# Kernel optimization log

Measured on AMD Instinct MI355X. Metric: run time of the kernel, lower is better.

Reference implementation:

```python
import jax, jax.numpy as jnp
import numpy as np

EPS = 1e-12


def conv3(x, W, b):
    # x: [B,C,H,W], W: [O,I,3,3] -> SAME conv, stride 1
    y = jax.lax.conv_general_dilated(x, W, (1, 1), 'SAME',
                                     dimension_numbers=('NCHW', 'OIHW', 'NCHW'))
    return y + b[None, :, None, None]


def unfold3(x):
    # torch F.unfold(kernel=3, padding=1): [B,C,H,W] -> [B, C*9, H*W]
    B, C, H, W = x.shape
    xp = jnp.pad(x, ((0, 0), (0, 0), (1, 1), (1, 1)))
    patches = jnp.stack([xp[:, :, i:i + H, j:j + W]
                         for i in range(3) for j in range(3)], axis=2)  # [B,C,9,H,W]
    return patches.reshape(B, C * 9, H * W)


def fold3(u, H, W):
    # torch F.fold(kernel=3, padding=1): [B, C*9, H*W] -> [B,C,H,W] (overlap-add)
    B = u.shape[0]
    C = u.shape[1] // 9
    p = u.reshape(B, C, 3, 3, H, W)
    out = jnp.zeros((B, C, H + 2, W + 2), u.dtype)
    for i in range(3):
        for j in range(3):
            out = out.at[:, :, i:i + H, j:j + W].add(p[:, :, i, j])
    return out[:, :, 1:-1, 1:-1]


def l2norm(v, axis):
    n = jnp.sqrt(jnp.sum(v * v, axis=axis, keepdims=True))
    return v / jnp.maximum(n, EPS)


def setup_inputs() -> dict:
    key = jax.random.key(0)
    ks = jax.random.split(key, 10)
    in_c, q_c = 64, 32
    B, H, W = 1, 96, 96
    s = 0.05
    return {
        'x':  jax.random.normal(ks[0], (B, in_c, H, W), jnp.float32),
        'W1': jax.random.normal(ks[1], (in_c, in_c, 3, 3), jnp.float32) * s,
        'b1': jax.random.normal(ks[2], (in_c,), jnp.float32) * s,
        'W2': jax.random.normal(ks[3], (in_c, in_c, 3, 3), jnp.float32) * s,
        'b2': jax.random.normal(ks[4], (in_c,), jnp.float32) * s,
        'Wq': jax.random.normal(ks[5], (q_c, in_c, 3, 3), jnp.float32) * s,
        'bq': jax.random.normal(ks[6], (q_c,), jnp.float32) * s,
        'Wk': jax.random.normal(ks[7], (q_c, in_c, 3, 3), jnp.float32) * s,
        'bk': jax.random.normal(ks[8], (q_c,), jnp.float32) * s,
    }


def reference(x, W1, b1, W2, b2, Wq, bq, Wk, bk):
    TOPK = 5
    B, C, H, W = x.shape
    L = H * W

    feature = jax.nn.relu(conv3(jax.nn.relu(conv3(x, W1, b1)), W2, b2))
    q = conv3(x, Wq, bq)
    k = conv3(x, Wk, bk)

    q_unfold = l2norm(unfold3(q), axis=1)                      # [B, Q9, L]
    k_unfold = l2norm(jnp.swapaxes(unfold3(k), 1, 2), axis=2)  # [B, L, Q9]

    R_qk = jnp.einsum('blc,bcm->blm', k_unfold, q_unfold)      # [B, L_k, L_q]

    # topk over dim=1 (key positions) for each query position
    vals, idxs = jax.lax.top_k(jnp.swapaxes(R_qk, 1, 2), TOPK)  # [B, L_q, K]
    R_maxs = jnp.swapaxes(vals, 1, 2)                           # [B, K, L]
    R_indexs = jnp.swapaxes(idxs, 1, 2)                         # [B, K, L]

    x_unfold = unfold3(x)                                       # [B, C*9, L]
    acc = jnp.zeros_like(x)
    for i in range(1, TOPK):
        idx = R_indexs[:, i, :][:, None, :]                     # [B,1,L]
        T_unfold = jnp.take_along_axis(x_unfold, idx, axis=2)   # [B, C*9, L]
        T = fold3(T_unfold, H, W) / 9.0
        S = R_maxs[:, i, :].reshape(B, 1, H, W)
        acc = acc + T * S
    y = feature + x + acc / float(TOPK - 1)
    return y
```

## Files before the change

### kernel.cpp

```cpp
#include <hip/hip_runtime.h>
#include <math.h>

#define HH 96
#define WW 96
#define LL 9216
#define D9 288
#define TOPK 5
#define NK 6
#define NCAND 8
#define KSPLIT 32
#define CPQ (KSPLIT * NK)
#define KEYS_PER_SPLIT (LL / KSPLIT)
#define PASSES (KEYS_PER_SPLIT / 32)
#define CHUNKS (32 * 36)
#define KROW 292

typedef short short8 __attribute__((ext_vector_type(8)));
typedef float f32x16 __attribute__((ext_vector_type(16)));

__device__ __forceinline__ float  asf(unsigned u) { union { unsigned u; float f; } a; a.u = u; return a.f; }
__device__ __forceinline__ unsigned asu(float f)  { union { float f; unsigned u; } a; a.f = f; return a.u; }

__device__ __forceinline__ unsigned short f2bf(float f) {
    unsigned u = asu(f);
    unsigned r = u + 0x7fff + ((u >> 16) & 1);
    return (unsigned short)(r >> 16);
}

template<int N>
__device__ __forceinline__ void ins_packed(float (&v)[N], float x) {
    #pragma unroll
    for (int s = 0; s < N; ++s) {
        float hi = fmaxf(v[s], x);
        x = fminf(v[s], x);
        v[s] = hi;
    }
}

__device__ __forceinline__ bool better_tb(float av, int ai, float bv, int bi) {
    return (av > bv) || (av == bv && ai < bi);
}

template<int N>
__device__ __forceinline__ void insert_tb(float (&v)[N], int (&ix)[N], float nv, int ni) {
    if (better_tb(nv, ni, v[N-1], ix[N-1])) {
        v[N-1] = nv; ix[N-1] = ni;
        #pragma unroll
        for (int s = N-1; s > 0; --s) {
            if (better_tb(v[s], ix[s], v[s-1], ix[s-1])) {
                float tv = v[s]; v[s] = v[s-1]; v[s-1] = tv;
                int ti = ix[s]; ix[s] = ix[s-1]; ix[s-1] = ti;
            }
        }
    }
}

__global__ __launch_bounds__(256) void conv_stage1_kernel(
    const float* __restrict__ x,
    const float* __restrict__ W1, const float* __restrict__ b1, float* __restrict__ c1,
    const float* __restrict__ Wq, const float* __restrict__ bq,
    const float* __restrict__ Wk, const float* __restrict__ bk,
    float* __restrict__ qq, float* __restrict__ kk)
{
    int pix = blockIdx.x * 256 + threadIdx.x;
    int y = pix / WW, x0 = pix % WW;

    int  offs[9]; bool msk[9];
    #pragma unroll
    for (int u = 0; u < 3; ++u)
        #pragma unroll
        for (int v = 0; v < 3; ++v) {
            int yy = y + u - 1, xx = x0 + v - 1;
            bool ok = ((unsigned)yy < 96u) && ((unsigned)xx < 96u);
            msk[u*3+v]  = ok;
            offs[u*3+v] = ok ? (yy*96 + xx) : 0;
        }

    int g = blockIdx.y;
    if (g < 8) {
        int co0 = g * 8;
        float acc[8];
        #pragma unroll
        for (int j = 0; j < 8; ++j) acc[j] = b1[co0 + j];
        #pragma unroll 2
        for (int ci = 0; ci < 64; ++ci) {
            const float* xp = x + (size_t)ci * LL;
            float v9[9];
            #pragma unroll
            for (int t = 0; t < 9; ++t) v9[t] = msk[t] ? xp[offs[t]] : 0.0f;
            const float* wb = W1 + (size_t)co0 * 64 * 9 + ci * 9;
            #pragma unroll
            for (int j = 0; j < 8; ++j) {
                const float* wp = wb + (size_t)j * 64 * 9;
                #pragma unroll
                for (int t = 0; t < 9; ++t) acc[j] = fmaf(v9[t], wp[t], acc[j]);
            }
        }
        #pragma unroll
        for (int j = 0; j < 8; ++j)
            c1[(size_t)(co0 + j) * LL + pix] = fmaxf(acc[j], 0.0f);
    } else {
        int co0 = (g - 8) * 4;
        float aq[4], ak[4];
        #pragma unroll
        for (int j = 0; j < 4; ++j) { aq[j] = bq[co0 + j]; ak[j] = bk[co0 + j]; }
        #pragma unroll 2
        for (int ci = 0; ci < 64; ++ci) {
            const float* xp = x + (size_t)ci * LL;
            float v9[9];
            #pragma unroll
            for (int t = 0; t < 9; ++t) v9[t] = msk[t] ? xp[offs[t]] : 0.0f;
            #pragma unroll
            for (int j = 0; j < 4; ++j) {
                const float* wpq = Wq + ((size_t)(co0 + j) * 64 + ci) * 9;
                const float* wpk = Wk + ((size_t)(co0 + j) * 64 + ci) * 9;
                #pragma unroll
                for (int t = 0; t < 9; ++t) {
                    aq[j] = fmaf(v9[t], wpq[t], aq[j]);
                    ak[j] = fmaf(v9[t], wpk[t], ak[j]);
                }
            }
        }
        #pragma unroll
        for (int j = 0; j < 4; ++j) {
            qq[(size_t)(co0 + j) * LL + pix] = aq[j];
            kk[(size_t)(co0 + j) * LL + pix] = ak[j];
        }
    }
}

__global__ __launch_bounds__(256) void conv3_co8_kernel(
    const float* __restrict__ in, const float* __restrict__ Wt,
    const float* __restrict__ bias, float* __restrict__ out)
{
    int co0 = blockIdx.y * 8;
    int pix = blockIdx.x * 256 + threadIdx.x;
    int y = pix / WW, x = pix % WW;

    int  offs[9]; bool msk[9];
    #pragma unroll
    for (int u = 0; u < 3; ++u)
        #pragma unroll
        for (int v = 0; v < 3; ++v) {
            int yy = y + u - 1, xx = x + v - 1;
            bool ok = ((unsigned)yy < 96u) && ((unsigned)xx < 96u);
            msk[u*3+v]  = ok;
            offs[u*3+v] = ok ? (yy*96 + xx) : 0;
        }

    float acc[8];
    #pragma unroll
    for (int j = 0; j < 8; ++j) acc[j] = bias[co0 + j];

    #pragma unroll 2
    for (int ci = 0; ci < 64; ++ci) {
        const float* xp = in + (size_t)ci * LL;
        float v9[9];
        #pragma unroll
        for (int t = 0; t < 9; ++t) v9[t] = msk[t] ? xp[offs[t]] : 0.0f;
        const float* wb = Wt + (size_t)co0 * 64 * 9 + ci * 9;
        #pragma unroll
        for (int j = 0; j < 8; ++j) {
            const float* wp = wb + (size_t)j * 64 * 9;
            #pragma unroll
            for (int t = 0; t < 9; ++t) acc[j] = fmaf(v9[t], wp[t], acc[j]);
        }
    }
    #pragma unroll
    for (int j = 0; j < 8; ++j)
        out[(size_t)(co0 + j) * LL + pix] = fmaxf(acc[j], 0.0f);
}

__global__ __launch_bounds__(256) void transpose_x_kernel(
    const float* __restrict__ x, float* __restrict__ xT)
{
    __shared__ float t[64][65];
    int pix0 = blockIdx.x * 64;
    int lp = threadIdx.x & 63, cg = threadIdx.x >> 6;
    #pragma unroll
    for (int cc = 0; cc < 16; ++cc) {
        int c = cg * 16 + cc;
        t[c][lp] = x[(size_t)c * LL + pix0 + lp];
    }
    __syncthreads();
    #pragma unroll
    for (int pp = 0; pp < 16; ++pp) {
        int pl = cg * 16 + pp;
        xT[(size_t)(pix0 + pl) * 64 + lp] = t[lp][pl];
    }
}

__global__ __launch_bounds__(256) void unfold_norm_kernel(
    const float* __restrict__ qq, float* __restrict__ q_f32, unsigned short* __restrict__ q_bf,
    const float* __restrict__ kk, float* __restrict__ k_f32, unsigned short* __restrict__ k_bf)
{
    const float* in; float* o32; unsigned short* obf;
    if (blockIdx.y == 0) { in = qq; o32 = q_f32; obf = q_bf; }
    else                 { in = kk; o32 = k_f32; obf = k_bf; }

    __shared__ float inv_s[32];
    int tid = threadIdx.x;
    int l0 = blockIdx.x * 32;

    {
        int pxl = tid >> 3, sub = tid & 7;
        int l = l0 + pxl;
        int y = l / WW, xx0 = l % WW;
        float ss = 0.0f;
        #pragma unroll
        for (int cc = 0; cc < 4; ++cc) {
            const float* xp = in + (size_t)(sub * 4 + cc) * LL;
            #pragma unroll
            for (int u = 0; u < 3; ++u) {
                int yy = y + u - 1;
                bool yok = (unsigned)yy < 96u;
                #pragma unroll
                for (int v = 0; v < 3; ++v) {
                    int xv = xx0 + v - 1;
                    float val = (yok && (unsigned)xv < 96u) ? xp[yy*96+xv] : 0.0f;
                    ss = fmaf(val, val, ss);
                }
            }
        }
        ss += __shfl_xor(ss, 1);
        ss += __shfl_xor(ss, 2);
        ss += __shfl_xor(ss, 4);
        if (sub == 0) inv_s[pxl] = 1.0f / fmaxf(sqrtf(ss), 1e-12f);
    }
    __syncthreads();

    #pragma unroll 1
    for (int it = 0; it < 9; ++it) {
        int e = it * 256 + tid;
        int pxl = e / 72, dc = e - pxl * 72;
        int l = l0 + pxl;
        int y = l / WW, xx0 = l % WW;
        float inv = inv_s[pxl];
        float4 o; float* op = &o.x;
        #pragma unroll
        for (int i = 0; i < 4; ++i) {
            int d = dc * 4 + i;
            int c = d / 9, rm = d - c * 9;
            int u = rm / 3, v = rm - u * 3;
            int yy = y + u - 1, xv = xx0 + v - 1;
            op[i] = ((unsigned)yy < 96u && (unsigned)xv < 96u)
                    ? in[(size_t)c * LL + yy*96 + xv] * inv : 0.0f;
        }
        *(float4*)(o32 + (size_t)l * D9 + dc * 4) = o;
        unsigned short b4[4];
        #pragma unroll
        for (int i = 0; i < 4; ++i) b4[i] = f2bf(op[i]);
        *(uint2*)(obf + (size_t)l * D9 + dc * 4) = *(uint2*)b4;
    }
}

__global__ __launch_bounds__(256, 2) void topk_mfma_kernel(
    const unsigned short* __restrict__ qn_bf, const unsigned short* __restrict__ kn_bf,
    float* __restrict__ valsQ)
{
    __shared__ unsigned short ks[2][32 * KROW];

    int tid  = threadIdx.x;
    int lane = tid & 63;
    int col = lane & 31, khalf = lane >> 5;
    int qtile = blockIdx.x >> 5;
    int split = blockIdx.x & 31;
    int q0w = qtile * 256 + (tid >> 6) * 64;
    int key0 = split * KEYS_PER_SPLIT;

    short8 qf[2][18];
    #pragma unroll
    for (int b = 0; b < 2; ++b) {
        const unsigned short* qrow = qn_bf + (size_t)(q0w + b*32 + col) * D9 + khalf * 8;
        #pragma unroll
        for (int dg = 0; dg < 18; ++dg)
            qf[b][dg] = *(const short8*)(qrow + dg * 16);
    }

    float lv0[NK], lv1[NK];
    #pragma unroll
    for (int s = 0; s < NK; ++s) { lv0[s] = -INFINITY; lv1[s] = -INFINITY; }

    const char* kg = (const char*)kn_bf;
    uint4 pre[5];

    #pragma unroll
    for (int c0 = 0; c0 < 5; ++c0) {
        int c = tid + c0 * 256;
        if (c < CHUNKS) {
            int key = c / 36, off = c - key * 36;
            pre[c0] = *(const uint4*)(kg + (size_t)(key0 + key) * 576 + off * 16);
        }
    }
    #pragma unroll
    for (int c0 = 0; c0 < 5; ++c0) {
        int c = tid + c0 * 256;
        if (c < CHUNKS) {
            int key = c / 36, off = c - key * 36;
            char* d = (char*)ks[0] + key * (KROW*2) + off * 16;
            *(uint2*)d       = *(uint2*)&pre[c0];
            *(uint2*)(d + 8) = *((uint2*)&pre[c0] + 1);
        }
    }
    __syncthreads();

    for (int p = 0; p < PASSES; ++p) {
        if (p + 1 < PASSES) {
            #pragma unroll
            for (int c0 = 0; c0 < 5; ++c0) {
                int c = tid + c0 * 256;
                if (c < CHUNKS) {
                    int key = c / 36, off = c - key * 36;
                    pre[c0] = *(const uint4*)(kg + (size_t)(key0 + (p+1)*32 + key) * 576 + off * 16);
                }
            }
        }

        f32x16 acc0 = {}, acc1 = {};
        const char* kb = (const char*)ks[p & 1] + (size_t)col * (KROW*2) + khalf * 16;
        #pragma unroll
        for (int dg = 0; dg < 18; ++dg) {
            short8 af;
            *(uint2*)&af       = *(const uint2*)(kb + dg * 32);
            *((uint2*)&af + 1) = *(const uint2*)(kb + dg * 32 + 8);
            acc0 = __builtin_amdgcn_mfma_f32_32x32x16_bf16(af, qf[0][dg], acc0, 0, 0, 0);
            acc1 = __builtin_amdgcn_mfma_f32_32x32x16_bf16(af, qf[1][dg], acc1, 0, 0, 0);
        }

        int lbase = p * 32 + 4 * khalf;
        #pragma unroll
        for (int r = 0; r < 16; ++r) {
            unsigned lkey = (unsigned)(lbase + (r & 3) + 8 * (r >> 2));
            float p0 = asf((asu(acc0[r]) & 0xFFFFFE00u) | lkey);
            if (p0 > lv0[NK-1]) ins_packed<NK>(lv0, p0);
            float p1 = asf((asu(acc1[r]) & 0xFFFFFE00u) | lkey);
            if (p1 > lv1[NK-1]) ins_packed<NK>(lv1, p1);
        }

        if (p + 1 < PASSES) {
            #pragma unroll
            for (int c0 = 0; c0 < 5; ++c0) {
                int c = tid + c0 * 256;
                if (c < CHUNKS) {
                    int key = c / 36, off = c - key * 36;
                    char* d = (char*)ks[(p+1) & 1] + key * (KROW*2) + off * 16;
                    *(uint2*)d       = *(uint2*)&pre[c0];
                    *(uint2*)(d + 8) = *((uint2*)&pre[c0] + 1);
                }
            }
        }
        __syncthreads();
    }

    #pragma unroll
    for (int b = 0; b < 2; ++b) {
        float* lv = b ? lv1 : lv0;
        float pv[NK];
        #pragma unroll
        for (int s = 0; s < NK; ++s) pv[s] = __shfl_xor(lv[s], 32);
        #pragma unroll
        for (int s = 0; s < NK; ++s) {
            float x = pv[s];
            #pragma unroll
            for (int t = 0; t < NK; ++t) {
                float hi = fmaxf(lv[t], x);
                x = fminf(lv[t], x);
                lv[t] = hi;
            }
        }
        if (lane < 32) {
            int q = q0w + b * 32 + col;
            float* vq = valsQ + (size_t)q * CPQ + split * NK;
            #pragma unroll
            for (int s = 0; s < NK; ++s) vq[s] = lv[s];
        }
    }
}

__global__ __launch_bounds__(256) void rerank_kernel(
    const float* __restrict__ valsQ,
    const float* __restrict__ qn_f32, const float* __restrict__ kn_f32,
    float* __restrict__ vals, int* __restrict__ idxs)
{
    int tid = threadIdx.x;
    int lane = tid & 63;
    int half = lane >> 5, l32 = lane & 31;
    int q = blockIdx.x * 8 + (tid >> 6) * 2 + half;

    const float* vq = valsQ + (size_t)q * CPQ + l32 * NK;
    float v[NK];
    #pragma unroll
    for (int s = 0; s < NK; ++s) v[s] = vq[s];

    int ckey[NCAND];
    #pragma unroll
    for (int it = 0; it < NCAND; ++it) {
        float cv = v[0];
        int cl = l32;
        #pragma unroll
        for (int st = 1; st < 32; st <<= 1) {
            float ov = __shfl_xor(cv, st);
            int ol = __shfl_xor(cl, st);
            if (ov > cv || (ov == cv && ol < cl)) { cv = ov; cl = ol; }
        }
        ckey[it] = cl * KEYS_PER_SPLIT + (int)(asu(cv) & 0x1FFu);
        if (cl == l32) {
            #pragma unroll
            for (int s = 0; s < NK-1; ++s) v[s] = v[s+1];
            v[NK-1] = -INFINITY;
        }
    }

    int r = l32 >> 2, part = l32 & 3;
    const float4* qr = (const float4*)(qn_f32 + (size_t)q * D9) + part * 18;
    const float4* kr = (const float4*)(kn_f32 + (size_t)ckey[r] * D9) + part * 18;
    float s0 = 0.f, s1 = 0.f, s2 = 0.f, s3 = 0.f;
    #pragma unroll
    for (int i2 = 0; i2 < 18; ++i2) {
        float4 a = qr[i2], b = kr[i2];
        s0 = fmaf(a.x, b.x, s0); s1 = fmaf(a.y, b.y, s1);
        s2 = fmaf(a.z, b.z, s2); s3 = fmaf(a.w, b.w, s3);
    }
    float sc = (s0 + s1) + (s2 + s3);
    sc += __shfl_xor(sc, 1);
    sc += __shfl_xor(sc, 2);

    float bv[TOPK]; int bi[TOPK];
    #pragma unroll
    for (int s = 0; s < TOPK; ++s) { bv[s] = -INFINITY; bi[s] = 0x7fffffff; }
    #pragma unroll
    for (int cc = 0; cc < NCAND; ++cc) {
        float sv = __shfl(sc, half * 32 + cc * 4);
        insert_tb<TOPK>(bv, bi, sv, ckey[cc]);
    }
    if (l32 == 0) {
        #pragma unroll
        for (int s = 0; s < TOPK; ++s) {
            vals[(size_t)s * LL + q] = bv[s];
            idxs[(size_t)s * LL + q] = bi[s];
        }
    }
}

__global__ __launch_bounds__(256) void gather_out_kernel(
    const float* __restrict__ xT, const float* __restrict__ feat,
    const float* __restrict__ vals, const int* __restrict__ idxs,
    float* __restrict__ out)
{
    int wave = threadIdx.x >> 6, lane = threadIdx.x & 63;
    int pix = blockIdx.x * 4 + wave;
    int y = pix / WW, x0 = pix - y * WW;
    float acc = 0.0f;
    #pragma unroll 1
    for (int s = 1; s < TOPK; ++s) {
        float S = vals[(size_t)s * LL + pix] * (1.0f/9.0f);
        #pragma unroll
        for (int i = 0; i < 3; ++i) {
            int qy = y + 1 - i;
            #pragma unroll
            for (int j = 0; j < 3; ++j) {
                int qx = x0 + 1 - j;
                if ((unsigned)qy < 96u && (unsigned)qx < 96u) {
                    int l = idxs[(size_t)s * LL + qy * WW + qx];
                    int yl = l / WW, xl = l - yl * WW;
                    int sy = yl + i - 1, sx = xl + j - 1;
                    if ((unsigned)sy < 96u && (unsigned)sx < 96u)
                        acc = fmaf(S, xT[(size_t)(sy * WW + sx) * 64 + lane], acc);
                }
            }
        }
    }
    out[(size_t)lane * LL + pix] = feat[(size_t)lane * LL + pix]
                                 + xT[(size_t)pix * 64 + lane] + acc * 0.25f;
}

extern "C" void kernel_launch(void* const* d_in, const int* in_sizes, int n_in,
                              void* d_out, int out_size, void* d_ws, size_t ws_size,
                              hipStream_t stream)
{
    (void)in_sizes; (void)n_in; (void)out_size; (void)ws_size;
    const float* x  = (const float*)d_in[0];
    const float* W1 = (const float*)d_in[1];
    const float* b1 = (const float*)d_in[2];
    const float* W2 = (const float*)d_in[3];
    const float* b2 = (const float*)d_in[4];
    const float* Wq = (const float*)d_in[5];
    const float* bq = (const float*)d_in[6];
    const float* Wk = (const float*)d_in[7];
    const float* bk = (const float*)d_in[8];
    float* out = (float*)d_out;

    char* p = (char*)d_ws;
    float* c1     = (float*)p;            p += (size_t)64 * LL * 4;
    float* feat   = (float*)p;            p += (size_t)64 * LL * 4;
    float* xT     = (float*)p;            p += (size_t)64 * LL * 4;
    float* qq     = (float*)p;            p += (size_t)32 * LL * 4;
    float* kk     = (float*)p;            p += (size_t)32 * LL * 4;
    float* qn_f32 = (float*)p;            p += (size_t)LL * D9 * 4;
    float* kn_f32 = (float*)p;            p += (size_t)LL * D9 * 4;
    unsigned short* qn_bf = (unsigned short*)p;  p += (size_t)LL * D9 * 2;
    unsigned short* kn_bf = (unsigned short*)p;  p += (size_t)LL * D9 * 2;
    float* valsQ  = (float*)p;            p += (size_t)LL * CPQ * 4;
    float* vals   = (float*)p;            p += (size_t)TOPK * LL * 4;
    int*   idxs   = (int*)p;              p += (size_t)TOPK * LL * 4;

    conv_stage1_kernel<<<dim3(36, 16), 256, 0, stream>>>(x, W1, b1, c1, Wq, bq, Wk, bk, qq, kk);
    unfold_norm_kernel<<<dim3(288, 2), 256, 0, stream>>>(qq, qn_f32, qn_bf, kk, kn_f32, kn_bf);
    topk_mfma_kernel<<<36 * KSPLIT, 256, 0, stream>>>(qn_bf, kn_bf, valsQ);
    conv3_co8_kernel<<<dim3(36, 8), 256, 0, stream>>>(c1, W2, b2, feat);
    transpose_x_kernel<<<144, 256, 0, stream>>>(x, xT);
    rerank_kernel<<<LL / 8, 256, 0, stream>>>(valsQ, qn_f32, kn_f32, vals, idxs);
    gather_out_kernel<<<LL / 4, 256, 0, stream>>>(xT, feat, vals, idxs, out);
}
```

Measured before the change: 358.3 us.

## Halve conv channel tiles, stage unfold tile in LDS, use med3 top-k insertion

The conv kernels now compute 4 output channels per thread instead of 8, doubling the grid so more blocks run across the CUs, at the cost of reloading inputs twice as often. The unfold/normalize kernel stages a 3-row halo tile of q/k into shared memory once, instead of issuing repeated bounds-checked global loads. The top-k insertion swaps the branchy max/min bubble for a branchless fmed3-based insert that runs on every candidate, removing divergence but always doing the full work.

```diff
diff --git a/kernel.cpp b/kernel.cpp
--- a/kernel.cpp
+++ b/kernel.cpp
@@ -28,13 +28,13 @@
 }
 
 template<int N>
-__device__ __forceinline__ void ins_packed(float (&v)[N], float x) {
-    #pragma unroll
-    for (int s = 0; s < N; ++s) {
-        float hi = fmaxf(v[s], x);
-        x = fminf(v[s], x);
-        v[s] = hi;
-    }
+__device__ __forceinline__ void ins_med3(float* v, float x) {
+    float nv[N];
+    nv[0] = fmaxf(v[0], x);
+    #pragma unroll
+    for (int s = 1; s < N; ++s) nv[s] = __builtin_amdgcn_fmed3f(v[s-1], v[s], x);
+    #pragma unroll
+    for (int s = 0; s < N; ++s) v[s] = nv[s];
 }
 
 __device__ __forceinline__ bool better_tb(float av, int ai, float bv, int bi) {
@@ -77,30 +77,30 @@
         }
 
     int g = blockIdx.y;
-    if (g < 8) {
-        int co0 = g * 8;
-        float acc[8];
-        #pragma unroll
-        for (int j = 0; j < 8; ++j) acc[j] = b1[co0 + j];
+    if (g < 16) {
+        int co0 = g * 4;
+        float acc[4];
+        #pragma unroll
+        for (int j = 0; j < 4; ++j) acc[j] = b1[co0 + j];
         #pragma unroll 2
         for (int ci = 0; ci < 64; ++ci) {
             const float* xp = x + (size_t)ci * LL;
             float v9[9];
             #pragma unroll
             for (int t = 0; t < 9; ++t) v9[t] = msk[t] ? xp[offs[t]] : 0.0f;
-            const float* wb = W1 + (size_t)co0 * 64 * 9 + ci * 9;
-            #pragma unroll
-            for (int j = 0; j < 8; ++j) {
+            const float* wb = W1 + ((size_t)co0 * 64 + ci) * 9;
+            #pragma unroll
+            for (int j = 0; j < 4; ++j) {
                 const float* wp = wb + (size_t)j * 64 * 9;
                 #pragma unroll
                 for (int t = 0; t < 9; ++t) acc[j] = fmaf(v9[t], wp[t], acc[j]);
             }
         }
         #pragma unroll
-        for (int j = 0; j < 8; ++j)
+        for (int j = 0; j < 4; ++j)
             c1[(size_t)(co0 + j) * LL + pix] = fmaxf(acc[j], 0.0f);
     } else {
-        int co0 = (g - 8) * 4;
+        int co0 = (g - 16) * 4;
         float aq[4], ak[4];
         #pragma unroll
         for (int j = 0; j < 4; ++j) { aq[j] = bq[co0 + j]; ak[j] = bk[co0 + j]; }
@@ -129,11 +129,11 @@
     }
 }
 
-__global__ __launch_bounds__(256) void conv3_co8_kernel(
+__global__ __launch_bounds__(256) void conv3_co4_kernel(
     const float* __restrict__ in, const float* __restrict__ Wt,
     const float* __restrict__ bias, float* __restrict__ out)
 {
-    int co0 = blockIdx.y * 8;
+    int co0 = blockIdx.y * 4;
     int pix = blockIdx.x * 256 + threadIdx.x;
     int y = pix / WW, x = pix % WW;
 
@@ -148,9 +148,9 @@
             offs[u*3+v] = ok ? (yy*96 + xx) : 0;
         }
 
-    float acc[8];
-    #pragma unroll
-    for (int j = 0; j < 8; ++j) acc[j] = bias[co0 + j];
+    float acc[4];
+    #pragma unroll
+    for (int j = 0; j < 4; ++j) acc[j] = bias[co0 + j];
 
     #pragma unroll 2
     for (int ci = 0; ci < 64; ++ci) {
@@ -158,16 +158,16 @@
         float v9[9];
         #pragma unroll
         for (int t = 0; t < 9; ++t) v9[t] = msk[t] ? xp[offs[t]] : 0.0f;
-        const float* wb = Wt + (size_t)co0 * 64 * 9 + ci * 9;
-        #pragma unroll
-        for (int j = 0; j < 8; ++j) {
+        const float* wb = Wt + ((size_t)co0 * 64 + ci) * 9;
+        #pragma unroll
+        for (int j = 0; j < 4; ++j) {
             const float* wp = wb + (size_t)j * 64 * 9;
             #pragma unroll
             for (int t = 0; t < 9; ++t) acc[j] = fmaf(v9[t], wp[t], acc[j]);
         }
     }
     #pragma unroll
-    for (int j = 0; j < 8; ++j)
+    for (int j = 0; j < 4; ++j)
         out[(size_t)(co0 + j) * LL + pix] = fmaxf(acc[j], 0.0f);
 }
 
@@ -198,29 +198,38 @@
     if (blockIdx.y == 0) { in = qq; o32 = q_f32; obf = q_bf; }
     else                 { in = kk; o32 = k_f32; obf = k_bf; }
 
+    __shared__ float tile[3][32][34];
     __shared__ float inv_s[32];
     int tid = threadIdx.x;
     int l0 = blockIdx.x * 32;
+    int y = l0 / WW, xb = l0 % WW;
+
+    #pragma unroll
+    for (int j = 0; j < 13; ++j) {
+        int f = j * 256 + tid;
+        if (f < 3 * 32 * 34) {
+            int col = f % 34, cc = (f / 34) & 31, r = f / (34 * 32);
+            int yy = y + r - 1, xv = xb + col - 1;
+            float val = ((unsigned)yy < 96u && (unsigned)xv < 96u)
+                        ? in[(size_t)cc * LL + yy * 96 + xv] : 0.0f;
+            tile[r][cc][col] = val;
+        }
+    }
+    __syncthreads();
 
     {
         int pxl = tid >> 3, sub = tid & 7;
-        int l = l0 + pxl;
-        int y = l / WW, xx0 = l % WW;
         float ss = 0.0f;
         #pragma unroll
         for (int cc = 0; cc < 4; ++cc) {
-            const float* xp = in + (size_t)(sub * 4 + cc) * LL;
-            #pragma unroll
-            for (int u = 0; u < 3; ++u) {
-                int yy = y + u - 1;
-                bool yok = (unsigned)yy < 96u;
+            int c = sub * 4 + cc;
+            #pragma unroll
+            for (int u = 0; u < 3; ++u)
                 #pragma unroll
                 for (int v = 0; v < 3; ++v) {
-                    int xv = xx0 + v - 1;
-                    float val = (yok && (unsigned)xv < 96u) ? xp[yy*96+xv] : 0.0f;
+                    float val = tile[u][c][pxl + v];
                     ss = fmaf(val, val, ss);
                 }
-            }
         }
         ss += __shfl_xor(ss, 1);
         ss += __shfl_xor(ss, 2);
@@ -234,7 +243,6 @@
         int e = it * 256 + tid;
         int pxl = e / 72, dc = e - pxl * 72;
         int l = l0 + pxl;
-        int y = l / WW, xx0 = l % WW;
         float inv = inv_s[pxl];
         float4 o; float* op = &o.x;
         #pragma unroll
@@ -242,9 +250,7 @@
             int d = dc * 4 + i;
             int c = d / 9, rm = d - c * 9;
             int u = rm / 3, v = rm - u * 3;
-            int yy = y + u - 1, xv = xx0 + v - 1;
-            op[i] = ((unsigned)yy < 96u && (unsigned)xv < 96u)
-                    ? in[(size_t)c * LL + yy*96 + xv] * inv : 0.0f;
+            op[i] = tile[u][c][pxl + v] * inv;
         }
         *(float4*)(o32 + (size_t)l * D9 + dc * 4) = o;
         unsigned short b4[4];
@@ -331,10 +337,8 @@
         #pragma unroll
         for (int r = 0; r < 16; ++r) {
             unsigned lkey = (unsigned)(lbase + (r & 3) + 8 * (r >> 2));
-            float p0 = asf((asu(acc0[r]) & 0xFFFFFE00u) | lkey);
-            if (p0 > lv0[NK-1]) ins_packed<NK>(lv0, p0);
-            float p1 = asf((asu(acc1[r]) & 0xFFFFFE00u) | lkey);
-            if (p1 > lv1[NK-1]) ins_packed<NK>(lv1, p1);
+            ins_med3<NK>(lv0, asf((asu(acc0[r]) & 0xFFFFFE00u) | lkey));
+            ins_med3<NK>(lv1, asf((asu(acc1[r]) & 0xFFFFFE00u) | lkey));
         }
 
         if (p + 1 < PASSES) {
@@ -359,15 +363,7 @@
         #pragma unroll
         for (int s = 0; s < NK; ++s) pv[s] = __shfl_xor(lv[s], 32);
         #pragma unroll
-        for (int s = 0; s < NK; ++s) {
-            float x = pv[s];
-            #pragma unroll
-            for (int t = 0; t < NK; ++t) {
-                float hi = fmaxf(lv[t], x);
-                x = fminf(lv[t], x);
-                lv[t] = hi;
-            }
-        }
+        for (int s = 0; s < NK; ++s) ins_med3<NK>(lv, pv[s]);
         if (lane < 32) {
             int q = q0w + b * 32 + col;
             float* vq = valsQ + (size_t)q * CPQ + split * NK;
@@ -504,10 +500,10 @@
     float* vals   = (float*)p;            p += (size_t)TOPK * LL * 4;
     int*   idxs   = (int*)p;              p += (size_t)TOPK * LL * 4;
 
-    conv_stage1_kernel<<<dim3(36, 16), 256, 0, stream>>>(x, W1, b1, c1, Wq, bq, Wk, bk, qq, kk);
+    conv_stage1_kernel<<<dim3(36, 24), 256, 0, stream>>>(x, W1, b1, c1, Wq, bq, Wk, bk, qq, kk);
     unfold_norm_kernel<<<dim3(288, 2), 256, 0, stream>>>(qq, qn_f32, qn_bf, kk, kn_f32, kn_bf);
     topk_mfma_kernel<<<36 * KSPLIT, 256, 0, stream>>>(qn_bf, kn_bf, valsQ);
-    conv3_co8_kernel<<<dim3(36, 8), 256, 0, stream>>>(c1, W2, b2, feat);
+    conv3_co4_kernel<<<dim3(36, 16), 256, 0, stream>>>(c1, W2, b2, feat);
     transpose_x_kernel<<<144, 256, 0, stream>>>(x, xT);
     rerank_kernel<<<LL / 8, 256, 0, stream>>>(valsQ, qn_f32, kn_f32, vals, idxs);
     gather_out_kernel<<<LL / 4, 256, 0, stream>>>(xT, feat, vals, idxs, out);
```

New measurement: 307.2 us. 14.3% less time.
